# Kernel optimization log

Hardware: AMD Instinct MI355X
Metric: run time of the kernel (lower is better)

## Reference

```python
import jax, jax.numpy as jnp
import numpy as np
import math

B, T, M, C, H = 2, 2048, 77, 512, 8
D = C // H  # head dim = 64


def setup_inputs() -> dict:
    key = jax.random.key(0)
    ks = jax.random.split(key, 20)
    s = 0.02
    inp = {
        "x": jax.random.normal(ks[0], (B, T, C), jnp.float32),
        "c": jax.random.normal(ks[1], (B, M, C), jnp.float32),
        # causal mask for self-attention (masked_fill where == 0)
        "attn_mask": jnp.tril(jnp.ones((T, T), jnp.int32))[None, None],
        "padding_mask": jnp.ones((B, M), jnp.int32),
    }
    names = ["Wq", "Wk", "Wv", "Wkc", "Wvc", "Wg1", "Wg2", "Wp"]
    for i, n in enumerate(names):
        inp[n] = jax.random.normal(ks[2 + i], (C, C), jnp.float32) * s
        inp["b" + n[1:]] = jnp.zeros((C,), jnp.float32)
    return inp


def _heads(t):
    # [B, S, C] -> [B, S, H, D]
    return t.reshape(t.shape[0], t.shape[1], H, D)


def reference(x, c, attn_mask, padding_mask,
              Wq, bq, Wk, bk, Wv, bv, Wkc, bkc, Wvc, bvc,
              Wg1, bg1, Wg2, bg2, Wp, bp):
    scale = 1.0 / math.sqrt(D)
    q = _heads(x @ Wq + bq)      # [B,T,H,D]
    k = _heads(x @ Wk + bk)      # [B,T,H,D]
    v = _heads(x @ Wv + bv)
    k_c = _heads(c @ Wkc + bkc)  # [B,M,H,D]
    v_c = _heads(c @ Wvc + bvc)

    # self-attention branch
    att = jnp.einsum("bthd,bshd->bhts", q, k) * scale   # [B,H,T,T]
    att = jnp.where(attn_mask == 0, -jnp.inf, att)
    att = jax.nn.softmax(att, axis=-1)
    y = jnp.einsum("bhts,bshd->bthd", att, v).reshape(B, T, C)

    # cross-attention branch to condition c
    att_c = jnp.einsum("bthd,bmhd->bhtm", q, k_c) * scale  # [B,H,T,M]
    att_c = jnp.where(padding_mask[:, None, None, :] == 0, -jnp.inf, att_c)
    att_c = jax.nn.softmax(att_c, axis=-1)
    y_c = jnp.einsum("bhtm,bmhd->bthd", att_c, v_c).reshape(B, T, C)

    # sigmoid gating fusion (note: gates cross-multiply branches, per source)
    gate_self = jax.nn.sigmoid(y @ Wg1 + bg1)
    gate_c = jax.nn.sigmoid(y_c @ Wg2 + bg2)
    y = gate_self * y_c + gate_c * y
    return y @ Wp + bp
```

## Files before the change

kernel.cpp:

```cpp
#include <hip/hip_runtime.h>
#include <hip/hip_bf16.h>
#include <math.h>

#define BB 2
#define TT 2048
#define MM 77
#define CC 512
#define HH 8
#define DD 64

typedef short bf16x8 __attribute__((ext_vector_type(8)));
typedef float f32x4  __attribute__((ext_vector_type(4)));

static __device__ __forceinline__ unsigned short f2bf(float x) {
    __hip_bfloat16 h = __float2bfloat16(x);
    return *reinterpret_cast<unsigned short*>(&h);
}
static __device__ __forceinline__ float bf2f(unsigned short u) {
    unsigned int v = ((unsigned int)u) << 16;
    return *reinterpret_cast<float*>(&v);
}

__global__ __launch_bounds__(256)
void wconv8(const float* __restrict__ w0, const float* __restrict__ w1,
            const float* __restrict__ w2, const float* __restrict__ w3,
            const float* __restrict__ w4, const float* __restrict__ w5,
            const float* __restrict__ w6, const float* __restrict__ w7,
            unsigned short* __restrict__ outbase)
{
    const float* W;
    switch (blockIdx.z) {
        case 0: W = w0; break; case 1: W = w1; break;
        case 2: W = w2; break; case 3: W = w3; break;
        case 4: W = w4; break; case 5: W = w5; break;
        case 6: W = w6; break; default: W = w7; break;
    }
    unsigned short* Wp = outbase + (size_t)blockIdx.z * 512 * 512;
    const int k0 = blockIdx.x * 64;
    const int n0 = blockIdx.y * 64;
    const int tid = threadIdx.x;
    __shared__ unsigned short t[64 * 72];

    #pragma unroll
    for (int it = 0; it < 4; ++it) {
        const int e = tid + 256 * it;
        const int r  = e >> 4;
        const int c4 = (e & 15) * 4;
        const float4 v = *(const float4*)(W + (size_t)(k0 + r) * 512 + n0 + c4);
        t[(c4 + 0) * 72 + r] = f2bf(v.x);
        t[(c4 + 1) * 72 + r] = f2bf(v.y);
        t[(c4 + 2) * 72 + r] = f2bf(v.z);
        t[(c4 + 3) * 72 + r] = f2bf(v.w);
    }
    __syncthreads();
    #pragma unroll
    for (int it = 0; it < 2; ++it) {
        const int e    = tid + 256 * it;
        const int gl   = e >> 7;
        const int ktl  = (e >> 6) & 1;
        const int lane = e & 63;
        const int l15  = lane & 15;
        const int q    = lane >> 4;
        const int4 v = *(const int4*)&t[(gl * 16 + l15) * 72 + ktl * 32 + q * 8];
        const int G  = (n0 >> 4) + gl;
        const int KT = (k0 >> 5) + ktl;
        *(int4*)(Wp + ((size_t)(G * 16 + KT) * 64 + lane) * 8) = v;
    }
}

__global__ __launch_bounds__(256)
void proj_all(const float* __restrict__ x, const float* __restrict__ cin,
              const unsigned short* __restrict__ Wt8,
              const float* __restrict__ bq, const float* __restrict__ bk,
              const float* __restrict__ bv, const float* __restrict__ bkc,
              const float* __restrict__ bvc,
              unsigned short* __restrict__ qb,
              unsigned short* __restrict__ vtb,
              unsigned short* __restrict__ kcb,
              unsigned short* __restrict__ vtcb)
{
    __shared__ unsigned short As[2 * 16 * 64 * 8];

    const int tid = threadIdx.x;
    int b = blockIdx.x;
    const float* Ap; const unsigned short* Wtp;
    const float *bb0, *bb1, *bb2;
    int row0, colb, N, isSelf;
    float oscale;
    if (b < 768) {
        isSelf = 1;
        row0 = (b & 127) * 32; colb = (b >> 7) * 256;
        Ap = x; Wtp = Wt8; N = BB * TT;
        oscale = 0.125f;
        bb0 = bq; bb1 = bk; bb2 = bv;
    } else {
        b -= 768; isSelf = 0;
        row0 = (b % 5) * 32; colb = (b / 5) * 256;
        Ap = cin; Wtp = Wt8 + 3 * 262144; N = BB * MM;
        oscale = 1.0f;
        bb0 = bkc; bb1 = bvc; bb2 = nullptr;
    }

    {
        const int r    = tid >> 3;
        const int rg   = r >> 4;
        const int l15r = r & 15;
        const int seg  = (tid & 7) * 64;
        const int gr   = row0 + r;
        unsigned short tmp[64];
        #pragma unroll
        for (int j = 0; j < 16; ++j) {
            float4 v = (gr < N) ? *(const float4*)(Ap + (size_t)gr * 512 + seg + j * 4)
                                : make_float4(0.f, 0.f, 0.f, 0.f);
            tmp[j*4+0] = f2bf(v.x); tmp[j*4+1] = f2bf(v.y);
            tmp[j*4+2] = f2bf(v.z); tmp[j*4+3] = f2bf(v.w);
        }
        #pragma unroll
        for (int jb = 0; jb < 8; ++jb) {
            const int k  = seg + jb * 8;
            const int kt = k >> 5;
            const int q  = (k >> 3) & 3;
            *(int4*)&As[((rg * 16 + kt) * 64 + q * 16 + l15r) * 8] = *(int4*)&tmp[jb*8];
        }
    }
    __syncthreads();

    const int wv   = tid >> 6;
    const int lane = tid & 63;
    const int l15  = lane & 15;
    const int quad = lane >> 4;
    const int wc   = colb + wv * 64;
    const int wcg  = wc >> 4;

    f32x4 acc[2][4];
    #pragma unroll
    for (int mi = 0; mi < 2; ++mi)
        #pragma unroll
        for (int ni = 0; ni < 4; ++ni) acc[mi][ni] = (f32x4){0.f, 0.f, 0.f, 0.f};

    bf16x8 b0v[4], b1v[4], b2v[4];
    #pragma unroll
    for (int ni = 0; ni < 4; ++ni) {
        b0v[ni] = *(const bf16x8*)(Wtp + (((size_t)(wcg + ni) * 16 + 0) << 9) + lane * 8);
        b1v[ni] = *(const bf16x8*)(Wtp + (((size_t)(wcg + ni) * 16 + 1) << 9) + lane * 8);
    }

    for (int kt = 0; kt < 16; ++kt) {
        if (kt + 2 < 16) {
            #pragma unroll
            for (int ni = 0; ni < 4; ++ni)
                b2v[ni] = *(const bf16x8*)(Wtp + (((size_t)(wcg + ni) * 16 + kt + 2) << 9) + lane * 8);
        }
        const bf16x8 a0 = *(const bf16x8*)&As[((0 * 16 + kt) * 64 + lane) * 8];
        const bf16x8 a1 = *(const bf16x8*)&As[((1 * 16 + kt) * 64 + lane) * 8];
        #pragma unroll
        for (int ni = 0; ni < 4; ++ni) {
            acc[0][ni] = __builtin_amdgcn_mfma_f32_16x16x32_bf16(a0, b0v[ni], acc[0][ni], 0, 0, 0);
            acc[1][ni] = __builtin_amdgcn_mfma_f32_16x16x32_bf16(a1, b0v[ni], acc[1][ni], 0, 0, 0);
        }
        #pragma unroll
        for (int ni = 0; ni < 4; ++ni) { b0v[ni] = b1v[ni]; b1v[ni] = b2v[ni]; }
    }

    const int which = wc >> 9;
    const float* bsel = (which == 0) ? bb0 : ((which == 1) ? bb1 : bb2);
    const float sc = (which == 0) ? oscale : 1.f;

    float bvv[4];
    #pragma unroll
    for (int ni = 0; ni < 4; ++ni)
        bvv[ni] = bsel[(wc + ni * 16 + l15) & 511];

    if (isSelf) {
        const int b_ = row0 >> 11;
        const int t0 = row0 & 2047;
        const int h  = (wc & 511) >> 6;
        __syncthreads();
        if (which < 2) {
            unsigned short* TL = (unsigned short*)As + wv * (32 * 72);
            #pragma unroll
            for (int mi = 0; mi < 2; ++mi)
                #pragma unroll
                for (int ni = 0; ni < 4; ++ni)
                    #pragma unroll
                    for (int reg = 0; reg < 4; ++reg) {
                        const int t = mi * 16 + quad * 4 + reg;
                        const int d = ni * 16 + l15;
                        TL[t * 72 + d] = f2bf((acc[mi][ni][reg] + bvv[ni]) * sc);
                    }
            unsigned short* dst = qb + (size_t)which * 2097152
                                + (((size_t)b_ * 8 + h) * 2048 + t0) * 64;
            #pragma unroll
            for (int it = 0; it < 4; ++it) {
                const int t = it * 8 + (lane >> 3);
                *(int4*)(dst + (size_t)t * 64 + (lane & 7) * 8)
                    = *(const int4*)&TL[t * 72 + (lane & 7) * 8];
            }
        } else {
            unsigned short* TL = (unsigned short*)As + wv * (64 * 40);
            #pragma unroll
            for (int mi = 0; mi < 2; ++mi)
                #pragma unroll
                for (int ni = 0; ni < 4; ++ni) {
                    ushort4 u;
                    u.x = f2bf(acc[mi][ni][0] + bvv[ni]);
                    u.y = f2bf(acc[mi][ni][1] + bvv[ni]);
                    u.z = f2bf(acc[mi][ni][2] + bvv[ni]);
                    u.w = f2bf(acc[mi][ni][3] + bvv[ni]);
                    const int d = ni * 16 + l15;
                    *(ushort4*)&TL[d * 40 + mi * 16 + quad * 4] = u;
                }
            unsigned short* dst = vtb + (((size_t)b_ * 8 + h) * 64) * 2048 + t0;
            #pragma unroll
            for (int it = 0; it < 4; ++it) {
                const int d = it * 16 + (lane >> 2);
                *(int4*)(dst + (size_t)d * 2048 + (lane & 3) * 8)
                    = *(const int4*)&TL[d * 40 + (lane & 3) * 8];
            }
        }
    } else {
        #pragma unroll
        for (int mi = 0; mi < 2; ++mi)
            #pragma unroll
            for (int reg = 0; reg < 4; ++reg) {
                const int row = row0 + mi * 16 + quad * 4 + reg;
                if (row >= N) continue;
                const int b_ = (row >= MM) ? 1 : 0;
                const int m_ = row - b_ * MM;
                #pragma unroll
                for (int ni = 0; ni < 4; ++ni) {
                    const float v = acc[mi][ni][reg] + bvv[ni];
                    const int cl = (wc + ni * 16 + l15) & 511;
                    const int hh = cl >> 6, d = cl & 63;
                    if (which == 0)
                        kcb[(((size_t)b_ * 8 + hh) * 77 + m_) * 64 + d] = f2bf(v);
                    else
                        vtcb[(((size_t)b_ * 8 + hh) * 64 + d) * 128 + m_] = f2bf(v);
                }
            }
        if (which == 1 && row0 == 0) {
            const int h0 = (colb - 512) >> 6;
            for (int e = tid; e < 2 * 4 * 64; e += 256) {
                const int d  = e & 63;
                const int hl = (e >> 6) & 3;
                const int bz = e >> 8;
                unsigned short* rp = vtcb + (((size_t)bz * 8 + h0 + hl) * 64 + d) * 128;
                rp[77] = 0; rp[78] = 0; rp[79] = 0;
                #pragma unroll
                for (int q8 = 80; q8 < 128; q8 += 8)
                    *(int4*)(rp + q8) = make_int4(0, 0, 0, 0);
            }
        }
    }
}

template<int ACT, int OUT, int AMODE>
__global__ __launch_bounds__(256)
void gemm_rs(const void* __restrict__ A0, const void* __restrict__ A1,
             const void* __restrict__ A2, const void* __restrict__ A3,
             const unsigned short* __restrict__ Wt,
             const float* __restrict__ b0, const float* __restrict__ b1,
             void* __restrict__ out0, void* __restrict__ out1,
             int N, int NC)
{
    __shared__ unsigned short As[2 * 16 * 64 * 8];

    const int tid  = threadIdx.x;
    const int z    = blockIdx.z;
    const int row0 = blockIdx.x * 32;
    const int colb = blockIdx.y * 256;
    const void* Ap = z ? A1 : A0;

    {
        const int r    = tid >> 3;
        const int rg   = r >> 4;
        const int l15r = r & 15;
        const int seg  = (tid & 7) * 64;
        const int gr   = row0 + r;
        unsigned short tmp[64];
        if (AMODE == 2) {
            #pragma unroll
            for (int jb = 0; jb < 8; ++jb) {
                unsigned short a[8], bq_[8], c[8], d[8];
                if (gr < N) {
                    const size_t off = (size_t)gr * 512 + seg + jb * 8;
                    *(int4*)a   = *(const int4*)((const unsigned short*)A0 + off);
                    *(int4*)bq_ = *(const int4*)((const unsigned short*)A1 + off);
                    *(int4*)c   = *(const int4*)((const unsigned short*)A2 + off);
                    *(int4*)d   = *(const int4*)((const unsigned short*)A3 + off);
                    #pragma unroll
                    for (int k = 0; k < 8; ++k)
                        tmp[jb*8+k] = f2bf(bf2f(a[k]) * bf2f(bq_[k]) + bf2f(c[k]) * bf2f(d[k]));
                } else {
                    #pragma unroll
                    for (int k = 0; k < 8; ++k) tmp[jb*8+k] = 0;
                }
            }
        } else {
            const unsigned short* Ab = (const unsigned short*)Ap;
            #pragma unroll
            for (int jb = 0; jb < 8; ++jb) {
                int4 v = (gr < N) ? *(const int4*)(Ab + (size_t)gr * 512 + seg + jb * 8)
                                  : make_int4(0, 0, 0, 0);
                *(int4*)&tmp[jb*8] = v;
            }
        }
        #pragma unroll
        for (int jb = 0; jb < 8; ++jb) {
            const int k  = seg + jb * 8;
            const int kt = k >> 5;
            const int q  = (k >> 3) & 3;
            *(int4*)&As[((rg * 16 + kt) * 64 + q * 16 + l15r) * 8] = *(int4*)&tmp[jb*8];
        }
    }
    __syncthreads();

    const int wv   = tid >> 6;
    const int lane = tid & 63;
    const int l15  = lane & 15;
    const int quad = lane >> 4;
    const int wc   = colb + wv * 64;
    const int wcg  = wc >> 4;

    f32x4 acc[2][4];
    #pragma unroll
    for (int mi = 0; mi < 2; ++mi)
        #pragma unroll
        for (int ni = 0; ni < 4; ++ni) acc[mi][ni] = (f32x4){0.f, 0.f, 0.f, 0.f};

    const unsigned short* Wz = Wt + (size_t)z * NC;

    bf16x8 b0v[4], b1v[4], b2v[4];
    #pragma unroll
    for (int ni = 0; ni < 4; ++ni) {
        b0v[ni] = *(const bf16x8*)(Wz + (((size_t)(wcg + ni) * 16 + 0) << 9) + lane * 8);
        b1v[ni] = *(const bf16x8*)(Wz + (((size_t)(wcg + ni) * 16 + 1) << 9) + lane * 8);
    }

    for (int kt = 0; kt < 16; ++kt) {
        if (kt + 2 < 16) {
            #pragma unroll
            for (int ni = 0; ni < 4; ++ni)
                b2v[ni] = *(const bf16x8*)(Wz + (((size_t)(wcg + ni) * 16 + kt + 2) << 9) + lane * 8);
        }
        const bf16x8 a0 = *(const bf16x8*)&As[((0 * 16 + kt) * 64 + lane) * 8];
        const bf16x8 a1 = *(const bf16x8*)&As[((1 * 16 + kt) * 64 + lane) * 8];
        #pragma unroll
        for (int ni = 0; ni < 4; ++ni) {
            acc[0][ni] = __builtin_amdgcn_mfma_f32_16x16x32_bf16(a0, b0v[ni], acc[0][ni], 0, 0, 0);
            acc[1][ni] = __builtin_amdgcn_mfma_f32_16x16x32_bf16(a1, b0v[ni], acc[1][ni], 0, 0, 0);
        }
        #pragma unroll
        for (int ni = 0; ni < 4; ++ni) { b0v[ni] = b1v[ni]; b1v[ni] = b2v[ni]; }
    }

    const float* bsel = ((OUT == 1) && z) ? b1 : b0;
    float bvv[4];
    #pragma unroll
    for (int ni = 0; ni < 4; ++ni)
        bvv[ni] = bsel[(wc + ni * 16 + l15) & 511];

    #pragma unroll
    for (int mi = 0; mi < 2; ++mi) {
        #pragma unroll
        for (int reg = 0; reg < 4; ++reg) {
            const int row = row0 + mi * 16 + quad * 4 + reg;
            if (row >= N) continue;
            #pragma unroll
            for (int ni = 0; ni < 4; ++ni) {
                float v = acc[mi][ni][reg] + bvv[ni];
                if (ACT == 1) v = 1.f / (1.f + __expf(-v));
                const int col = wc + ni * 16 + l15;
                if (OUT == 0) {
                    ((float*)out0)[(size_t)row * 512 + col] = v;
                } else {
                    unsigned short* dst = (unsigned short*)(z ? out1 : out0);
                    dst[(size_t)row * 512 + col] = f2bf(v);
                }
            }
        }
    }
}

__global__ __launch_bounds__(256)
void attn_all(const unsigned short* __restrict__ Qh,
              const unsigned short* __restrict__ Kh,
              const unsigned short* __restrict__ Vth,
              unsigned short* __restrict__ yout,
              const unsigned short* __restrict__ Kch,
              const unsigned short* __restrict__ Vtch,
              unsigned short* __restrict__ ycout)
{
    int lin = blockIdx.x;
    int causal, S_kv, W, bh, qt;
    const unsigned short *Kb, *Vb;
    unsigned short* outp;
    if (lin < 512) {
        causal = 1; S_kv = TT; W = TT;
        bh = (lin & 7) | (((lin >> 3) & 1) << 3);
        const int qtr = lin >> 4;
        qt = (qtr < 16) ? (31 - qtr) : (qtr - 16);
        Kb = Kh + (size_t)bh * S_kv * 64;
        Vb = Vth + (size_t)bh * 64 * W;
        outp = yout;
    } else {
        lin -= 512;
        causal = 0; S_kv = MM; W = 128;
        bh = (lin & 7) | (((lin >> 3) & 1) << 3);
        qt = lin >> 4;
        Kb = Kch + (size_t)bh * S_kv * 64;
        Vb = Vtch + (size_t)bh * 64 * W;
        outp = ycout;
    }
    const int n_kt = causal ? (qt + 1) : 2;

    const int tid  = threadIdx.x;
    const int wv   = tid >> 6;
    const int lane = tid & 63;
    const int l15  = lane & 15;
    const int quad = lane >> 4;

    __shared__ unsigned short Ks[64 * 80];
    __shared__ unsigned short Vs[64 * 80];
    __shared__ unsigned short PT[4 * 16 * 72];

    const int t0 = qt * 64 + wv * 16;
    const unsigned short* qptr = Qh + ((size_t)bh * TT + t0 + l15) * 64 + quad * 8;
    const bf16x8 qb0 = *(const bf16x8*)(qptr);
    const bf16x8 qb1 = *(const bf16x8*)(qptr + 32);

    f32x4 Oacc[4];
    #pragma unroll
    for (int dt = 0; dt < 4; ++dt) Oacc[dt] = (f32x4){0.f, 0.f, 0.f, 0.f};
    float l = 0.f;

    int4 kR[2], vR[2];
    {
        #pragma unroll
        for (int it = 0; it < 2; ++it) {
            const int e = tid + 256 * it;
            const int row = e >> 3, blk = e & 7;
            kR[it] = (row < S_kv)
                ? *(const int4*)(Kb + (size_t)row * 64 + blk * 8) : make_int4(0,0,0,0);
            vR[it] = (blk * 8 < W)
                ? *(const int4*)(Vb + (size_t)row * W + blk * 8) : make_int4(0,0,0,0);
        }
        #pragma unroll
        for (int it = 0; it < 2; ++it) {
            const int e = tid + 256 * it;
            const int row = e >> 3, blk = e & 7;
            *(int4*)&Ks[row * 80 + ((blk ^ (row & 7)) * 8)] = kR[it];
            *(int4*)&Vs[row * 80 + ((blk ^ (row & 7)) * 8)] = vR[it];
        }
    }
    __syncthreads();

    for (int kt = 0; kt < n_kt; ++kt) {
        const int s0 = kt * 64;

        if (kt + 1 < n_kt) {
            const int s1 = (kt + 1) * 64;
            #pragma unroll
            for (int it = 0; it < 2; ++it) {
                const int e = tid + 256 * it;
                const int row = e >> 3, blk = e & 7;
                const int s = s1 + row;
                kR[it] = (s < S_kv)
                    ? *(const int4*)(Kb + (size_t)s * 64 + blk * 8) : make_int4(0,0,0,0);
                vR[it] = (s1 + blk * 8 < W)
                    ? *(const int4*)(Vb + (size_t)row * W + s1 + blk * 8) : make_int4(0,0,0,0);
            }
        }

        f32x4 sacc[4];
        __builtin_amdgcn_s_setprio(1);
        #pragma unroll
        for (int mt = 0; mt < 4; ++mt) {
            const int krow = 16 * mt + l15;
            const bf16x8 ka0 = *(const bf16x8*)&Ks[krow * 80 + (((quad    ) ^ (krow & 7)) * 8)];
            const bf16x8 ka1 = *(const bf16x8*)&Ks[krow * 80 + (((quad + 4) ^ (krow & 7)) * 8)];
            sacc[mt] = (f32x4){0.f, 0.f, 0.f, 0.f};
            sacc[mt] = __builtin_amdgcn_mfma_f32_16x16x32_bf16(ka0, qb0, sacc[mt], 0, 0, 0);
            sacc[mt] = __builtin_amdgcn_mfma_f32_16x16x32_bf16(ka1, qb1, sacc[mt], 0, 0, 0);
        }
        __builtin_amdgcn_s_setprio(0);

        float sv[16];
        #pragma unroll
        for (int mt = 0; mt < 4; ++mt)
            #pragma unroll
            for (int reg = 0; reg < 4; ++reg)
                sv[mt * 4 + reg] = sacc[mt][reg];

        const bool cmask = (causal && kt == qt);
        if (cmask || (s0 + 64 > S_kv)) {
            const int lim = cmask ? (t0 + l15) : 0x7fffffff;
            #pragma unroll
            for (int mt = 0; mt < 4; ++mt)
                #pragma unroll
                for (int reg = 0; reg < 4; ++reg) {
                    const int kg = s0 + 16 * mt + quad * 4 + reg;
                    if (kg > lim || kg >= S_kv) sv[mt * 4 + reg] = -INFINITY;
                }
        }

        float p[16], psum = 0.f;
        #pragma unroll
        for (int i = 0; i < 16; ++i) { p[i] = __expf(sv[i]); psum += p[i]; }
        psum += __shfl_xor(psum, 16);
        psum += __shfl_xor(psum, 32);
        l += psum;

        unsigned short* ptw = &PT[wv * 16 * 72 + l15 * 72];
        #pragma unroll
        for (int mt = 0; mt < 4; ++mt) {
            ushort4 u;
            u.x = f2bf(p[mt * 4 + 0]); u.y = f2bf(p[mt * 4 + 1]);
            u.z = f2bf(p[mt * 4 + 2]); u.w = f2bf(p[mt * 4 + 3]);
            *(ushort4*)(ptw + 16 * mt + quad * 4) = u;
        }
        const bf16x8 pb0 = *(const bf16x8*)(ptw + quad * 8);
        const bf16x8 pb1 = *(const bf16x8*)(ptw + quad * 8 + 32);

        __builtin_amdgcn_s_setprio(1);
        #pragma unroll
        for (int dt = 0; dt < 4; ++dt) {
            const int vrow = 16 * dt + l15;
            const bf16x8 va0 = *(const bf16x8*)&Vs[vrow * 80 + (((quad    ) ^ (vrow & 7)) * 8)];
            const bf16x8 va1 = *(const bf16x8*)&Vs[vrow * 80 + (((quad + 4) ^ (vrow & 7)) * 8)];
            Oacc[dt] = __builtin_amdgcn_mfma_f32_16x16x32_bf16(va0, pb0, Oacc[dt], 0, 0, 0);
            Oacc[dt] = __builtin_amdgcn_mfma_f32_16x16x32_bf16(va1, pb1, Oacc[dt], 0, 0, 0);
        }
        __builtin_amdgcn_s_setprio(0);

        if (kt + 1 < n_kt) {
            __syncthreads();
            #pragma unroll
            for (int it = 0; it < 2; ++it) {
                const int e = tid + 256 * it;
                const int row = e >> 3, blk = e & 7;
                *(int4*)&Ks[row * 80 + ((blk ^ (row & 7)) * 8)] = kR[it];
                *(int4*)&Vs[row * 80 + ((blk ^ (row & 7)) * 8)] = vR[it];
            }
            __syncthreads();
        }
    }

    const int b = bh >> 3, h = bh & 7;
    const float inv_l = 1.f / l;
    const int t = t0 + l15;
    unsigned short* ob = outp + ((size_t)b * TT + t) * CC + h * DD + quad * 4;
    #pragma unroll
    for (int dt = 0; dt < 4; ++dt) {
        ushort4 u;
        u.x = f2bf(Oacc[dt][0] * inv_l);
        u.y = f2bf(Oacc[dt][1] * inv_l);
        u.z = f2bf(Oacc[dt][2] * inv_l);
        u.w = f2bf(Oacc[dt][3] * inv_l);
        *(ushort4*)(ob + 16 * dt) = u;
    }
}

extern "C" void kernel_launch(void* const* d_in, const int* in_sizes, int n_in,
                              void* d_out, int out_size, void* d_ws, size_t ws_size,
                              hipStream_t stream)
{
    const float* x   = (const float*)d_in[0];
    const float* cin = (const float*)d_in[1];
    const float* Wq  = (const float*)d_in[4];   const float* bq  = (const float*)d_in[5];
    const float* Wk  = (const float*)d_in[6];   const float* bk  = (const float*)d_in[7];
    const float* Wv  = (const float*)d_in[8];   const float* bv  = (const float*)d_in[9];
    const float* Wkc = (const float*)d_in[10];  const float* bkc = (const float*)d_in[11];
    const float* Wvc = (const float*)d_in[12];  const float* bvc = (const float*)d_in[13];
    const float* Wg1 = (const float*)d_in[14];  const float* bg1 = (const float*)d_in[15];
    const float* Wg2 = (const float*)d_in[16];  const float* bg2 = (const float*)d_in[17];
    const float* Wp  = (const float*)d_in[18];  const float* bp  = (const float*)d_in[19];

    float* out = (float*)d_out;
    char*  w   = (char*)d_ws;
    const size_t MB = 1024 * 1024;

    unsigned short* Wt8  = (unsigned short*)(w);
    unsigned short* qb   = (unsigned short*)(w + 4  * MB);
    unsigned short* vtb  = (unsigned short*)(w + 16 * MB);
    unsigned short* yb   = (unsigned short*)(w + 20 * MB);
    unsigned short* ycb  = (unsigned short*)(w + 24 * MB);
    unsigned short* g1b  = (unsigned short*)(w + 28 * MB);
    unsigned short* g2b  = (unsigned short*)(w + 32 * MB);
    unsigned short* kcb  = (unsigned short*)(w + 40 * MB);
    unsigned short* vtcb = (unsigned short*)(w + 40 * MB + 512 * 1024);

    const dim3 blk(256);

    wconv8<<<dim3(8, 8, 8), blk, 0, stream>>>(Wq, Wk, Wv, Wkc, Wvc, Wg1, Wg2, Wp, Wt8);

    proj_all<<<dim3(788), blk, 0, stream>>>(
        x, cin, Wt8, bq, bk, bv, bkc, bvc, qb, vtb, kcb, vtcb);

    attn_all<<<dim3(1024), blk, 0, stream>>>(
        qb, qb + 2097152, vtb, yb, kcb, vtcb, ycb);

    gemm_rs<1, 1, 0><<<dim3(128, 2, 2), blk, 0, stream>>>(
        yb, ycb, nullptr, nullptr, Wt8 + 5 * 262144, bg1, bg2, g1b, g2b,
        BB * TT, 262144);

    gemm_rs<0, 0, 2><<<dim3(128, 2), blk, 0, stream>>>(
        g1b, ycb, g2b, yb, Wt8 + 7 * 262144, bp, nullptr, out, nullptr,
        BB * TT, 0);
}
```

Measured before the change: 201.6 us.

## Fuse gate GEMMs, gating combine, and output projection into one kernel

Replaces the two gemm_rs launches (sigmoid gate GEMMs, then a combine plus output projection) with one kernel, gates_final. Each block loads 16 rows of y and y_c into shared memory once, computes both gates in registers, forms the gated mix, writes it back to shared memory and runs the output projection. This removes the bf16 gate buffers in global memory and one launch. In exchange each block covers only 16 rows, so 256 blocks each stream all three weight matrices, and each wave runs a longer chain of MFMA work.

Measured after the change: 189.9 us. 1.06x faster.

```diff
diff --git a/kernel.cpp b/kernel.cpp
--- a/kernel.cpp
+++ b/kernel.cpp
@@ -249,134 +249,6 @@
                 #pragma unroll
                 for (int q8 = 80; q8 < 128; q8 += 8)
                     *(int4*)(rp + q8) = make_int4(0, 0, 0, 0);
-            }
-        }
-    }
-}
-
-template<int ACT, int OUT, int AMODE>
-__global__ __launch_bounds__(256)
-void gemm_rs(const void* __restrict__ A0, const void* __restrict__ A1,
-             const void* __restrict__ A2, const void* __restrict__ A3,
-             const unsigned short* __restrict__ Wt,
-             const float* __restrict__ b0, const float* __restrict__ b1,
-             void* __restrict__ out0, void* __restrict__ out1,
-             int N, int NC)
-{
-    __shared__ unsigned short As[2 * 16 * 64 * 8];
-
-    const int tid  = threadIdx.x;
-    const int z    = blockIdx.z;
-    const int row0 = blockIdx.x * 32;
-    const int colb = blockIdx.y * 256;
-    const void* Ap = z ? A1 : A0;
-
-    {
-        const int r    = tid >> 3;
-        const int rg   = r >> 4;
-        const int l15r = r & 15;
-        const int seg  = (tid & 7) * 64;
-        const int gr   = row0 + r;
-        unsigned short tmp[64];
-        if (AMODE == 2) {
-            #pragma unroll
-            for (int jb = 0; jb < 8; ++jb) {
-                unsigned short a[8], bq_[8], c[8], d[8];
-                if (gr < N) {
-                    const size_t off = (size_t)gr * 512 + seg + jb * 8;
-                    *(int4*)a   = *(const int4*)((const unsigned short*)A0 + off);
-                    *(int4*)bq_ = *(const int4*)((const unsigned short*)A1 + off);
-                    *(int4*)c   = *(const int4*)((const unsigned short*)A2 + off);
-                    *(int4*)d   = *(const int4*)((const unsigned short*)A3 + off);
-                    #pragma unroll
-                    for (int k = 0; k < 8; ++k)
-                        tmp[jb*8+k] = f2bf(bf2f(a[k]) * bf2f(bq_[k]) + bf2f(c[k]) * bf2f(d[k]));
-                } else {
-                    #pragma unroll
-                    for (int k = 0; k < 8; ++k) tmp[jb*8+k] = 0;
-                }
-            }
-        } else {
-            const unsigned short* Ab = (const unsigned short*)Ap;
-            #pragma unroll
-            for (int jb = 0; jb < 8; ++jb) {
-                int4 v = (gr < N) ? *(const int4*)(Ab + (size_t)gr * 512 + seg + jb * 8)
-                                  : make_int4(0, 0, 0, 0);
-                *(int4*)&tmp[jb*8] = v;
-            }
-        }
-        #pragma unroll
-        for (int jb = 0; jb < 8; ++jb) {
-            const int k  = seg + jb * 8;
-            const int kt = k >> 5;
-            const int q  = (k >> 3) & 3;
-            *(int4*)&As[((rg * 16 + kt) * 64 + q * 16 + l15r) * 8] = *(int4*)&tmp[jb*8];
-        }
-    }
-    __syncthreads();
-
-    const int wv   = tid >> 6;
-    const int lane = tid & 63;
-    const int l15  = lane & 15;
-    const int quad = lane >> 4;
-    const int wc   = colb + wv * 64;
-    const int wcg  = wc >> 4;
-
-    f32x4 acc[2][4];
-    #pragma unroll
-    for (int mi = 0; mi < 2; ++mi)
-        #pragma unroll
-        for (int ni = 0; ni < 4; ++ni) acc[mi][ni] = (f32x4){0.f, 0.f, 0.f, 0.f};
-
-    const unsigned short* Wz = Wt + (size_t)z * NC;
-
-    bf16x8 b0v[4], b1v[4], b2v[4];
-    #pragma unroll
-    for (int ni = 0; ni < 4; ++ni) {
-        b0v[ni] = *(const bf16x8*)(Wz + (((size_t)(wcg + ni) * 16 + 0) << 9) + lane * 8);
-        b1v[ni] = *(const bf16x8*)(Wz + (((size_t)(wcg + ni) * 16 + 1) << 9) + lane * 8);
-    }
-
-    for (int kt = 0; kt < 16; ++kt) {
-        if (kt + 2 < 16) {
-            #pragma unroll
-            for (int ni = 0; ni < 4; ++ni)
-                b2v[ni] = *(const bf16x8*)(Wz + (((size_t)(wcg + ni) * 16 + kt + 2) << 9) + lane * 8);
-        }
-        const bf16x8 a0 = *(const bf16x8*)&As[((0 * 16 + kt) * 64 + lane) * 8];
-        const bf16x8 a1 = *(const bf16x8*)&As[((1 * 16 + kt) * 64 + lane) * 8];
-        #pragma unroll
-        for (int ni = 0; ni < 4; ++ni) {
-            acc[0][ni] = __builtin_amdgcn_mfma_f32_16x16x32_bf16(a0, b0v[ni], acc[0][ni], 0, 0, 0);
-            acc[1][ni] = __builtin_amdgcn_mfma_f32_16x16x32_bf16(a1, b0v[ni], acc[1][ni], 0, 0, 0);
-        }
-        #pragma unroll
-        for (int ni = 0; ni < 4; ++ni) { b0v[ni] = b1v[ni]; b1v[ni] = b2v[ni]; }
-    }
-
-    const float* bsel = ((OUT == 1) && z) ? b1 : b0;
-    float bvv[4];
-    #pragma unroll
-    for (int ni = 0; ni < 4; ++ni)
-        bvv[ni] = bsel[(wc + ni * 16 + l15) & 511];
-
-    #pragma unroll
-    for (int mi = 0; mi < 2; ++mi) {
-        #pragma unroll
-        for (int reg = 0; reg < 4; ++reg) {
-            const int row = row0 + mi * 16 + quad * 4 + reg;
-            if (row >= N) continue;
-            #pragma unroll
-            for (int ni = 0; ni < 4; ++ni) {
-                float v = acc[mi][ni][reg] + bvv[ni];
-                if (ACT == 1) v = 1.f / (1.f + __expf(-v));
-                const int col = wc + ni * 16 + l15;
-                if (OUT == 0) {
-                    ((float*)out0)[(size_t)row * 512 + col] = v;
-                } else {
-                    unsigned short* dst = (unsigned short*)(z ? out1 : out0);
-                    dst[(size_t)row * 512 + col] = f2bf(v);
-                }
             }
         }
     }
@@ -561,6 +433,164 @@
     }
 }
 
+__global__ __launch_bounds__(256)
+void gates_final(const unsigned short* __restrict__ yb,
+                 const unsigned short* __restrict__ ycb,
+                 const unsigned short* __restrict__ Wt8,
+                 const float* __restrict__ bg1, const float* __restrict__ bg2,
+                 const float* __restrict__ bp,
+                 float* __restrict__ out)
+{
+    __shared__ unsigned short Ay[16 * 512];
+    __shared__ unsigned short Ac[16 * 512];
+
+    const int tid  = threadIdx.x;
+    const int row0 = blockIdx.x * 16;
+
+    {
+        const int r   = tid >> 4;
+        const int seg = (tid & 15) * 32;
+        const int kt  = seg >> 5;
+        const unsigned short* ys = yb  + (size_t)(row0 + r) * 512 + seg;
+        const unsigned short* cs = ycb + (size_t)(row0 + r) * 512 + seg;
+        #pragma unroll
+        for (int jb = 0; jb < 4; ++jb) {
+            *(int4*)&Ay[(kt * 64 + jb * 16 + r) * 8] = *(const int4*)(ys + jb * 8);
+            *(int4*)&Ac[(kt * 64 + jb * 16 + r) * 8] = *(const int4*)(cs + jb * 8);
+        }
+    }
+    __syncthreads();
+
+    const int wv   = tid >> 6;
+    const int lane = tid & 63;
+    const int l15  = lane & 15;
+    const int quad = lane >> 4;
+    const int wc   = wv * 128;
+
+    const unsigned short* W1 = Wt8 + 5 * 262144;
+    const unsigned short* W2 = Wt8 + 6 * 262144;
+    const unsigned short* W3 = Wt8 + 7 * 262144;
+
+    unsigned int g1p[16], g2p[16];
+
+    #pragma unroll
+    for (int gg = 0; gg < 2; ++gg) {
+        const unsigned short* Wg = gg ? W2 : W1;
+        const unsigned short* Ax = gg ? Ac : Ay;
+        const float* bg = gg ? bg2 : bg1;
+        #pragma unroll
+        for (int half = 0; half < 2; ++half) {
+            const int wcg = (wc >> 4) + half * 4;
+            f32x4 acc[4];
+            #pragma unroll
+            for (int ni = 0; ni < 4; ++ni) acc[ni] = (f32x4){0.f, 0.f, 0.f, 0.f};
+            bf16x8 b0v[4], b1v[4], b2v[4];
+            #pragma unroll
+            for (int ni = 0; ni < 4; ++ni) {
+                b0v[ni] = *(const bf16x8*)(Wg + (((size_t)(wcg + ni) * 16 + 0) << 9) + lane * 8);
+                b1v[ni] = *(const bf16x8*)(Wg + (((size_t)(wcg + ni) * 16 + 1) << 9) + lane * 8);
+            }
+            for (int kt = 0; kt < 16; ++kt) {
+                if (kt + 2 < 16) {
+                    #pragma unroll
+                    for (int ni = 0; ni < 4; ++ni)
+                        b2v[ni] = *(const bf16x8*)(Wg + (((size_t)(wcg + ni) * 16 + kt + 2) << 9) + lane * 8);
+                }
+                const bf16x8 a = *(const bf16x8*)&Ax[(kt * 64 + lane) * 8];
+                #pragma unroll
+                for (int ni = 0; ni < 4; ++ni)
+                    acc[ni] = __builtin_amdgcn_mfma_f32_16x16x32_bf16(a, b0v[ni], acc[ni], 0, 0, 0);
+                #pragma unroll
+                for (int ni = 0; ni < 4; ++ni) { b0v[ni] = b1v[ni]; b1v[ni] = b2v[ni]; }
+            }
+            #pragma unroll
+            for (int ni = 0; ni < 4; ++ni) {
+                const float bv = bg[wc + (half * 4 + ni) * 16 + l15];
+                float s[4];
+                #pragma unroll
+                for (int reg = 0; reg < 4; ++reg) {
+                    const float v = acc[ni][reg] + bv;
+                    s[reg] = 1.f / (1.f + __expf(-v));
+                }
+                const unsigned int p01 = (unsigned int)f2bf(s[0]) | ((unsigned int)f2bf(s[1]) << 16);
+                const unsigned int p23 = (unsigned int)f2bf(s[2]) | ((unsigned int)f2bf(s[3]) << 16);
+                if (gg == 0) {
+                    g1p[half * 8 + ni * 2 + 0] = p01;
+                    g1p[half * 8 + ni * 2 + 1] = p23;
+                } else {
+                    g2p[half * 8 + ni * 2 + 0] = p01;
+                    g2p[half * 8 + ni * 2 + 1] = p23;
+                }
+            }
+        }
+    }
+
+    unsigned short zp[32];
+    #pragma unroll
+    for (int ni = 0; ni < 8; ++ni) {
+        #pragma unroll
+        for (int reg = 0; reg < 4; ++reg) {
+            const int r = quad * 4 + reg;
+            const int c = wc + ni * 16 + l15;
+            const int addr = ((c >> 5) * 64 + ((c >> 3) & 3) * 16 + r) * 8 + (c & 7);
+            const float yv = bf2f(Ay[addr]);
+            const float cv = bf2f(Ac[addr]);
+            const unsigned int p1 = g1p[ni * 2 + (reg >> 1)];
+            const unsigned int p2 = g2p[ni * 2 + (reg >> 1)];
+            const unsigned short g1v = (reg & 1) ? (unsigned short)(p1 >> 16) : (unsigned short)(p1 & 0xffff);
+            const unsigned short g2v = (reg & 1) ? (unsigned short)(p2 >> 16) : (unsigned short)(p2 & 0xffff);
+            zp[ni * 4 + reg] = f2bf(bf2f(g1v) * cv + bf2f(g2v) * yv);
+        }
+    }
+    __syncthreads();
+    #pragma unroll
+    for (int ni = 0; ni < 8; ++ni)
+        #pragma unroll
+        for (int reg = 0; reg < 4; ++reg) {
+            const int r = quad * 4 + reg;
+            const int c = wc + ni * 16 + l15;
+            Ay[((c >> 5) * 64 + ((c >> 3) & 3) * 16 + r) * 8 + (c & 7)] = zp[ni * 4 + reg];
+        }
+    __syncthreads();
+
+    #pragma unroll
+    for (int half = 0; half < 2; ++half) {
+        const int wcg = (wc >> 4) + half * 4;
+        f32x4 acc[4];
+        #pragma unroll
+        for (int ni = 0; ni < 4; ++ni) acc[ni] = (f32x4){0.f, 0.f, 0.f, 0.f};
+        bf16x8 b0v[4], b1v[4], b2v[4];
+        #pragma unroll
+        for (int ni = 0; ni < 4; ++ni) {
+            b0v[ni] = *(const bf16x8*)(W3 + (((size_t)(wcg + ni) * 16 + 0) << 9) + lane * 8);
+            b1v[ni] = *(const bf16x8*)(W3 + (((size_t)(wcg + ni) * 16 + 1) << 9) + lane * 8);
+        }
+        for (int kt = 0; kt < 16; ++kt) {
+            if (kt + 2 < 16) {
+                #pragma unroll
+                for (int ni = 0; ni < 4; ++ni)
+                    b2v[ni] = *(const bf16x8*)(W3 + (((size_t)(wcg + ni) * 16 + kt + 2) << 9) + lane * 8);
+            }
+            const bf16x8 a = *(const bf16x8*)&Ay[(kt * 64 + lane) * 8];
+            #pragma unroll
+            for (int ni = 0; ni < 4; ++ni)
+                acc[ni] = __builtin_amdgcn_mfma_f32_16x16x32_bf16(a, b0v[ni], acc[ni], 0, 0, 0);
+            #pragma unroll
+            for (int ni = 0; ni < 4; ++ni) { b0v[ni] = b1v[ni]; b1v[ni] = b2v[ni]; }
+        }
+        #pragma unroll
+        for (int ni = 0; ni < 4; ++ni) {
+            const int col = wc + (half * 4 + ni) * 16 + l15;
+            const float bv = bp[col];
+            #pragma unroll
+            for (int reg = 0; reg < 4; ++reg) {
+                const int row = row0 + quad * 4 + reg;
+                out[(size_t)row * 512 + col] = acc[ni][reg] + bv;
+            }
+        }
+    }
+}
+
 extern "C" void kernel_launch(void* const* d_in, const int* in_sizes, int n_in,
                               void* d_out, int out_size, void* d_ws, size_t ws_size,
                               hipStream_t stream)
@@ -585,8 +615,6 @@
     unsigned short* vtb  = (unsigned short*)(w + 16 * MB);
     unsigned short* yb   = (unsigned short*)(w + 20 * MB);
     unsigned short* ycb  = (unsigned short*)(w + 24 * MB);
-    unsigned short* g1b  = (unsigned short*)(w + 28 * MB);
-    unsigned short* g2b  = (unsigned short*)(w + 32 * MB);
     unsigned short* kcb  = (unsigned short*)(w + 40 * MB);
     unsigned short* vtcb = (unsigned short*)(w + 40 * MB + 512 * 1024);
 
@@ -600,11 +628,6 @@
     attn_all<<<dim3(1024), blk, 0, stream>>>(
         qb, qb + 2097152, vtb, yb, kcb, vtcb, ycb);
 
-    gemm_rs<1, 1, 0><<<dim3(128, 2, 2), blk, 0, stream>>>(
-        yb, ycb, nullptr, nullptr, Wt8 + 5 * 262144, bg1, bg2, g1b, g2b,
-        BB * TT, 262144);
-
-    gemm_rs<0, 0, 2><<<dim3(128, 2), blk, 0, stream>>>(
-        g1b, ycb, g2b, yb, Wt8 + 7 * 262144, bp, nullptr, out, nullptr,
-        BB * TT, 0);
+    gates_final<<<dim3(256), blk, 0, stream>>>(
+        yb, ycb, Wt8, bg1, bg2, bp, out);
 }
```
